# Optimization experiments

Measured on AMD Instinct MI355X. Metric: run time of the kernel, lower is better.

Reference implementation:

```python
import jax, jax.numpy as jnp
import numpy as np

N = 100000   # nodes
E = 1600000  # edges (before self-loops)
G = 64       # graphs in batch
IN = 8
H = 4        # heads
EPS_BN = 1e-5

def setup_inputs() -> dict:
    key = jax.random.key(0)
    ks = jax.random.split(key, 30)
    def nrm(k, shape, s=0.1):
        return jax.random.normal(k, shape, dtype=jnp.float32) * s
    inp = {}
    inp['x'] = nrm(ks[0], (N, IN), 1.0)
    inp['edge_index'] = jax.random.randint(ks[1], (2, E), 0, N)
    inp['batch'] = jnp.sort(jax.random.randint(ks[2], (N,), 0, G))
    # GATConv 1: 8 -> 64, 4 heads (concat=False)
    inp['W1'] = nrm(ks[3], (IN, H * 64)); inp['aS1'] = nrm(ks[4], (H, 64)); inp['aD1'] = nrm(ks[5], (H, 64)); inp['b1'] = jnp.zeros((64,), jnp.float32)
    inp['g1'] = jnp.ones((64,), jnp.float32); inp['be1'] = jnp.zeros((64,), jnp.float32)
    # GATConv 2: 64 -> 64
    inp['W2'] = nrm(ks[6], (64, H * 64)); inp['aS2'] = nrm(ks[7], (H, 64)); inp['aD2'] = nrm(ks[8], (H, 64)); inp['b2'] = jnp.zeros((64,), jnp.float32)
    inp['g2'] = jnp.ones((64,), jnp.float32); inp['be2'] = jnp.zeros((64,), jnp.float32)
    # GATConv 3: 64 -> 32
    inp['W3'] = nrm(ks[9], (64, H * 32)); inp['aS3'] = nrm(ks[10], (H, 32)); inp['aD3'] = nrm(ks[11], (H, 32)); inp['b3'] = jnp.zeros((32,), jnp.float32)
    inp['g3'] = jnp.ones((32,), jnp.float32); inp['be3'] = jnp.zeros((32,), jnp.float32)
    # predictor MLP 32 -> 16 -> 1
    inp['Wp1'] = nrm(ks[12], (32, 16)); inp['bp1'] = jnp.zeros((16,), jnp.float32)
    inp['Wp2'] = nrm(ks[13], (16, 1)); inp['bp2'] = jnp.zeros((1,), jnp.float32)
    return inp

def gat_layer(x, src, dst, W, a_src, a_dst, bias, D):
    # x: [N, Fin]; src/dst: [E'] (self-loops included). PyG GATConv semantics.
    h = (x @ W).reshape(N, H, D)                       # [N,H,D]
    alpha_s = jnp.einsum('nhd,hd->nh', h, a_src)       # [N,H]
    alpha_d = jnp.einsum('nhd,hd->nh', h, a_dst)
    e = jax.nn.leaky_relu(alpha_s[src] + alpha_d[dst], 0.2)  # [E',H]
    # segment softmax over incoming edges of each target node
    m = jax.ops.segment_max(e, dst, num_segments=N)
    e = jnp.exp(e - m[dst])
    s = jax.ops.segment_sum(e, dst, num_segments=N)
    alpha = e / (s[dst] + 1e-16)                       # [E',H]
    out = jax.ops.segment_sum(h[src] * alpha[:, :, None], dst, num_segments=N)  # [N,H,D]
    return out.mean(axis=1) + bias                     # concat=False -> head mean

def batch_norm(x, gamma, beta):
    m = x.mean(0)
    v = x.var(0)
    return (x - m) * jax.lax.rsqrt(v + EPS_BN) * gamma + beta

def reference(x, edge_index, batch,
              W1, aS1, aD1, b1, g1, be1,
              W2, aS2, aD2, b2, g2, be2,
              W3, aS3, aD3, b3, g3, be3,
              Wp1, bp1, Wp2, bp2):
    loop = jnp.arange(N)
    src = jnp.concatenate([edge_index[0], loop])  # add self loops (PyG default)
    dst = jnp.concatenate([edge_index[1], loop])
    h = jax.nn.relu(gat_layer(x, src, dst, W1, aS1, aD1, b1, 64))
    h = batch_norm(h, g1, be1)
    h = jax.nn.relu(gat_layer(h, src, dst, W2, aS2, aD2, b2, 64))
    h = batch_norm(h, g2, be2)
    h = jax.nn.relu(gat_layer(h, src, dst, W3, aS3, aD3, b3, 32))
    h = batch_norm(h, g3, be3)
    # global mean pool over graphs
    cnt = jax.ops.segment_sum(jnp.ones((N,), h.dtype), batch, num_segments=G)
    pooled = jax.ops.segment_sum(h, batch, num_segments=G) / jnp.maximum(cnt, 1.0)[:, None]
    hid = jax.nn.relu(pooled @ Wp1 + bp1)
    return hid @ Wp2 + bp2  # [G,1]
```

## Files before the change

### kernel.cpp

```cpp
#include <hip/hip_runtime.h>
#include <hip/hip_fp16.h>

#define N_NODES 100000
#define N_EDGES 1600000
#define EP (N_EDGES + N_NODES)
#define NG 64
#define NH 4
#define POOL_NPB 256
#define BSHIFT 7
#define BNODES 128
#define NBUCK 782
#define BCAP 3072
#define BCHUNK 4096
#define NBLK2 (N_NODES / 16)
#define NBLK1 (N_NODES / 32)
#define NBINS 64

static inline int cdiv(int a, int b) { return (a + b - 1) / b; }

typedef _Float16 half8 __attribute__((ext_vector_type(8)));
typedef float f32x4 __attribute__((ext_vector_type(4)));

__device__ __forceinline__ float lrelu(float x) { return x >= 0.f ? x : 0.2f * x; }

__global__ __launch_bounds__(256) void k_bucket(const int* __restrict__ ei,
                                                int* __restrict__ gCursor,
                                                unsigned int* __restrict__ pairs) {
  __shared__ int cnt[NBUCK];
  __shared__ int base[NBUCK];
  int tid = threadIdx.x;
  for (int b = tid; b < NBUCK; b += 256) cnt[b] = 0;
  __syncthreads();
  int e0 = blockIdx.x * BCHUNK;
  unsigned int stV[16];
  int stB[16];
#pragma unroll
  for (int i = 0; i < 16; i++) {
    int e = e0 + i * 256 + tid;
    stB[i] = -1;
    if (e < EP) {
      int d, s;
      if (e < N_EDGES) {
        d = __builtin_nontemporal_load(&ei[N_EDGES + e]);
        s = __builtin_nontemporal_load(&ei[e]);
      } else {
        d = s = e - N_EDGES;
      }
      int b = d >> BSHIFT;
      stV[i] = ((unsigned int)s << BSHIFT) | (unsigned int)(d & (BNODES - 1));
      stB[i] = b;
      atomicAdd(&cnt[b], 1);
    }
  }
  __syncthreads();
  for (int b = tid; b < NBUCK; b += 256) {
    base[b] = atomicAdd(&gCursor[b], cnt[b]);
    cnt[b] = 0;
  }
  __syncthreads();
#pragma unroll
  for (int i = 0; i < 16; i++) {
    if (stB[i] >= 0) {
      int r = atomicAdd(&cnt[stB[i]], 1);
      pairs[base[stB[i]] + r] = stV[i];
    }
  }
}

__global__ __launch_bounds__(1024) void k_bscan(const int* __restrict__ gCursor,
                                                int* __restrict__ bstart) {
  __shared__ int sh[1024];
  int t = threadIdx.x;
  int v = (t < NBUCK) ? (gCursor[t] - t * BCAP) : 0;
  sh[t] = v;
  __syncthreads();
  for (int off = 1; off < 1024; off <<= 1) {
    int add = (t >= off) ? sh[t - off] : 0;
    __syncthreads();
    sh[t] += add;
    __syncthreads();
  }
  if (t < NBUCK) {
    bstart[t] = sh[t] - v;
    if (t == NBUCK - 1) bstart[NBUCK] = sh[t];
  }
}

__global__ __launch_bounds__(256) void k_build(const unsigned int* __restrict__ pairs,
                                               const int* __restrict__ bstart,
                                               int* __restrict__ indptr, int* __restrict__ esrc,
                                               int* __restrict__ ghist) {
  __shared__ int cnt[BNODES];
  __shared__ int exc[BNODES];
  __shared__ int ptr[BNODES];
  __shared__ int dh[NBINS];
  __shared__ int eLds[BCAP];
  int b = blockIdx.x;
  int tid = threadIdx.x;
  int obase = bstart[b];
  int nE = bstart[b + 1] - obase;
  int pbase = b * BCAP;
  if (tid < BNODES) cnt[tid] = 0;
  if (tid >= BNODES && tid < BNODES + NBINS) dh[tid - BNODES] = 0;
  __syncthreads();
  unsigned int stV[12];
#pragma unroll
  for (int i = 0; i < 12; i++) {
    int idx = i * 256 + tid;
    stV[i] = 0xFFFFFFFFu;
    if (idx < nE) {
      unsigned int v = pairs[pbase + idx];
      stV[i] = v;
      atomicAdd(&cnt[v & (BNODES - 1)], 1);
    }
  }
  __syncthreads();
  if (tid < BNODES) ptr[tid] = cnt[tid];
  __syncthreads();
  for (int off = 1; off < BNODES; off <<= 1) {
    int add = (tid < BNODES && tid >= off) ? ptr[tid - off] : 0;
    __syncthreads();
    if (tid < BNODES) ptr[tid] += add;
    __syncthreads();
  }
  if (tid < BNODES) {
    exc[tid] = ptr[tid] - cnt[tid];
    int n = (b << BSHIFT) + tid;
    if (n < N_NODES) {
      indptr[n] = obase + exc[tid];
      atomicAdd(&dh[min(cnt[tid], NBINS - 1)], 1);
    }
    cnt[tid] = 0;
  }
  if (b == NBUCK - 1 && tid == 0) indptr[N_NODES] = bstart[NBUCK];
  __syncthreads();
  if (tid < NBINS && dh[tid]) atomicAdd(&ghist[tid], dh[tid]);
#pragma unroll
  for (int i = 0; i < 12; i++) {
    if (stV[i] != 0xFFFFFFFFu) {
      int ln = stV[i] & (BNODES - 1);
      int r = atomicAdd(&cnt[ln], 1);
      eLds[exc[ln] + r] = (int)(stV[i] >> BSHIFT);
    }
  }
  __syncthreads();
  for (int idx = tid; idx < nE; idx += 256) esrc[obase + idx] = eLds[idx];
}

__global__ void k_dscan(const int* __restrict__ ghist, int* __restrict__ binCur) {
  if (threadIdx.x == 0) {
    int acc = 0;
    for (int b = 0; b < NBINS; b++) {
      binCur[b] = acc;
      acc += ghist[b];
    }
  }
}

__global__ __launch_bounds__(256) void k_dscat(const int* __restrict__ indptr,
                                               int* __restrict__ binCur,
                                               int* __restrict__ perm) {
  __shared__ int cnt[NBINS];
  __shared__ int base[NBINS];
  int t = threadIdx.x;
  if (t < NBINS) cnt[t] = 0;
  __syncthreads();
  int binr[2], nr[2];
#pragma unroll
  for (int i = 0; i < 2; i++) {
    int n = blockIdx.x * 512 + i * 256 + t;
    binr[i] = -1;
    if (n < N_NODES) {
      int deg = indptr[n + 1] - indptr[n];
      binr[i] = min(deg, NBINS - 1);
      nr[i] = n;
      atomicAdd(&cnt[binr[i]], 1);
    }
  }
  __syncthreads();
  if (t < NBINS) {
    base[t] = cnt[t] ? atomicAdd(&binCur[t], cnt[t]) : 0;
    cnt[t] = 0;
  }
  __syncthreads();
#pragma unroll
  for (int i = 0; i < 2; i++) {
    if (binr[i] >= 0) {
      int r = atomicAdd(&cnt[binr[i]], 1);
      perm[base[binr[i]] + r] = nr[i];
    }
  }
}

template <int FIN, int D>
__device__ void wvec_impl(const float* __restrict__ W, const float* __restrict__ aS,
                          const float* __restrict__ aD, float* __restrict__ wS,
                          float* __restrict__ wD, int t) {
  if (t >= 4 * FIN) return;
  int h = t / FIN, k = t % FIN;
  float ss = 0.f, dd = 0.f;
  for (int d = 0; d < D; d++) {
    float w = W[k * (4 * D) + h * D + d];
    ss = fmaf(w, aS[h * D + d], ss);
    dd = fmaf(w, aD[h * D + d], dd);
  }
  wS[h * FIN + k] = ss;
  wD[h * FIN + k] = dd;
}

template <int D>
__device__ void wcvt_frag(const float* __restrict__ W, __half* __restrict__ wf, int frag, int l) {
  constexpr int NCT = D / 16;
  int kt = frag / NCT, ct = frag % NCT;
  half8 v;
#pragma unroll
  for (int j = 0; j < 8; j++) {
    int kk = kt * 32 + (l >> 4) * 8 + j;
    int k = kk >> 2, h = kk & 3;
    v[j] = (_Float16)W[k * (4 * D) + h * D + ct * 16 + (l & 15)];
  }
  *(half8*)(wf + (size_t)frag * 512 + l * 8) = v;
}

__global__ __launch_bounds__(256) void k_prep(const float* W1, const float* aS1, const float* aD1,
                                              const float* W2, const float* aS2, const float* aD2,
                                              const float* W3, const float* aS3, const float* aD3,
                                              float* wS1, float* wD1, float* wS2, float* wD2,
                                              float* wS3, float* wD3,
                                              __half* wf1, __half* wf2, __half* wf3,
                                              int* gCursor) {
  int b = blockIdx.x, t = threadIdx.x;
  int f = t >> 6, l = t & 63;
  if (b == 0) wvec_impl<8, 64>(W1, aS1, aD1, wS1, wD1, t);
  else if (b == 1) wvec_impl<64, 64>(W2, aS2, aD2, wS2, wD2, t);
  else if (b == 2) wvec_impl<64, 32>(W3, aS3, aD3, wS3, wD3, t);
  else if (b == 3) wcvt_frag<64>(W1, wf1, f, l);
  else if (b < 12) wcvt_frag<64>(W2, wf2, (b - 4) * 4 + f, l);
  else if (b < 16) wcvt_frag<32>(W3, wf3, (b - 12) * 4 + f, l);
  else {
    int idx = (b - 16) * 256 + t;
    if (idx < NBUCK) gCursor[idx] = idx * BCAP;
  }
}

__global__ void k_attdots1(const float* __restrict__ x, const float* __restrict__ wS,
                           const float* __restrict__ wD, float4* __restrict__ as4,
                           float4* __restrict__ ad4) {
  int n = blockIdx.x * blockDim.x + threadIdx.x;
  if (n >= N_NODES) return;
  float4 s = {0, 0, 0, 0}, d = {0, 0, 0, 0};
#pragma unroll
  for (int k = 0; k < 8; k++) {
    float xv = x[(size_t)n * 8 + k];
    s.x = fmaf(xv, wS[k], s.x);
    s.y = fmaf(xv, wS[8 + k], s.y);
    s.z = fmaf(xv, wS[16 + k], s.z);
    s.w = fmaf(xv, wS[24 + k], s.w);
    d.x = fmaf(xv, wD[k], d.x);
    d.y = fmaf(xv, wD[8 + k], d.y);
    d.z = fmaf(xv, wD[16 + k], d.z);
    d.w = fmaf(xv, wD[24 + k], d.w);
  }
  as4[n] = s;
  ad4[n] = d;
}

__global__ __launch_bounds__(256) void k_dots(const __half* __restrict__ t16,
                                              const float* __restrict__ scale,
                                              const float* __restrict__ shift,
                                              const float* __restrict__ wS,
                                              const float* __restrict__ wD,
                                              float4* __restrict__ as4, float4* __restrict__ ad4) {
  int lane = threadIdx.x & 63;
  int n = blockIdx.x * 4 + (threadIdx.x >> 6);
  if (n >= N_NODES) return;
  float v = fmaf(__half2float(t16[(size_t)n * 64 + lane]), scale[lane], shift[lane]);
  float p0 = v * wS[lane], p1 = v * wS[64 + lane], p2 = v * wS[128 + lane], p3 = v * wS[192 + lane];
  float q0 = v * wD[lane], q1 = v * wD[64 + lane], q2 = v * wD[128 + lane], q3 = v * wD[192 + lane];
#pragma unroll
  for (int off = 32; off; off >>= 1) {
    p0 += __shfl_xor(p0, off); p1 += __shfl_xor(p1, off);
    p2 += __shfl_xor(p2, off); p3 += __shfl_xor(p3, off);
    q0 += __shfl_xor(q0, off); q1 += __shfl_xor(q1, off);
    q2 += __shfl_xor(q2, off); q3 += __shfl_xor(q3, off);
  }
  if (lane == 0) {
    as4[n] = make_float4(p0, p1, p2, p3);
    ad4[n] = make_float4(q0, q1, q2, q3);
  }
}

__global__ __launch_bounds__(256) void k_aggp1(const int* __restrict__ indptr,
                                               const int* __restrict__ perm,
                                               const int* __restrict__ esrc,
                                               const float* __restrict__ xg,
                                               const float4* __restrict__ as4,
                                               const float4* __restrict__ ad4,
                                               const __half* __restrict__ wfrag,
                                               const float* __restrict__ bias,
                                               __half* __restrict__ out16,
                                               float* __restrict__ part) {
  constexpr int GL = 8, NPW = 8, WB = NPW * (GL + 1);
  __shared__ int sOff[4 * WB];
  __shared__ float4 sW[4 * WB];
  __shared__ __align__(16) __half aT[32 * 40];
  int tid = threadIdx.x;
  int lane = tid & 63;
  int wv = tid >> 6;
  int q = lane & 7;
  int g = lane >> 3;
  int row = wv * 8 + g;
  int n = perm[blockIdx.x * 32 + row];
  int e0 = indptr[n], e1 = indptr[n + 1];
  float4 ad = ad4[n];
  int lbase = wv * WB + g * (GL + 1);
  const char* xb = (const char*)xg + q * 4;
  float s0 = 0.f, s1 = 0.f, s2 = 0.f, s3 = 0.f;
  float a0 = 0.f, a1 = 0.f, a2 = 0.f, a3 = 0.f;
  for (int c = e0; c < e1; c += GL) {
    int nc = min(GL, e1 - c);
    float w0 = 0.f, w1 = 0.f, w2 = 0.f, w3 = 0.f;
    int sB = 0;
    if (q < nc) {
      int sidx = esrc[c + q];
      float4 av = as4[sidx];
      w0 = __expf(lrelu(av.x + ad.x));
      w1 = __expf(lrelu(av.y + ad.y));
      w2 = __expf(lrelu(av.z + ad.z));
      w3 = __expf(lrelu(av.w + ad.w));
      sB = sidx << 5;
    }
    s0 += w0; s1 += w1; s2 += w2; s3 += w3;
    sOff[lbase + q] = sB;
    sW[lbase + q] = make_float4(w0, w1, w2, w3);
    __builtin_amdgcn_wave_barrier();
    for (int i = 0; i < nc; ++i) {
      float4 w = sW[lbase + i];
      float xv = *(const float*)(xb + sOff[lbase + i]);
      a0 = fmaf(w.x, xv, a0);
      a1 = fmaf(w.y, xv, a1);
      a2 = fmaf(w.z, xv, a2);
      a3 = fmaf(w.w, xv, a3);
    }
    __builtin_amdgcn_wave_barrier();
  }
#pragma unroll
  for (int off = 1; off < GL; off <<= 1) {
    s0 += __shfl_xor(s0, off);
    s1 += __shfl_xor(s1, off);
    s2 += __shfl_xor(s2, off);
    s3 += __shfl_xor(s3, off);
  }
  float r0 = 1.f / (s0 + 1e-16f), r1 = 1.f / (s1 + 1e-16f);
  float r2 = 1.f / (s2 + 1e-16f), r3 = 1.f / (s3 + 1e-16f);
  __half2 p01 = __floats2half2_rn(a0 * r0, a1 * r1);
  __half2 p23 = __floats2half2_rn(a2 * r2, a3 * r3);
  uint2 pk = make_uint2(*(unsigned*)&p01, *(unsigned*)&p23);
  *(uint2*)&aT[row * 40 + q * 4] = pk;
  __syncthreads();
  int ct = wv;
  int m = lane & 15, kg = lane >> 4;
  half8 bv = *(const half8*)(wfrag + ((size_t)ct * 64 + lane) * 8);
  float bvs = bias[ct * 16 + m];
  float psum = 0.f, psq = 0.f;
#pragma unroll
  for (int tt = 0; tt < 2; tt++) {
    half8 avf = *(const half8*)&aT[(tt * 16 + m) * 40 + kg * 8];
    f32x4 cacc = (f32x4){0.f, 0.f, 0.f, 0.f};
    cacc = __builtin_amdgcn_mfma_f32_16x16x32_f16(avf, bv, cacc, 0, 0, 0);
#pragma unroll
    for (int j = 0; j < 4; j++) {
      int nr = perm[blockIdx.x * 32 + tt * 16 + kg * 4 + j];
      float ov = fmaxf(fmaf(cacc[j], 0.25f, bvs), 0.f);
      out16[(size_t)nr * 64 + ct * 16 + m] = __float2half(ov);
      psum += ov;
      psq = fmaf(ov, ov, psq);
    }
  }
  psum += __shfl_xor(psum, 16); psum += __shfl_xor(psum, 32);
  psq += __shfl_xor(psq, 16); psq += __shfl_xor(psq, 32);
  if (kg == 0) {
    part[(size_t)blockIdx.x * 128 + ct * 16 + m] = psum;
    part[(size_t)blockIdx.x * 128 + 64 + ct * 16 + m] = psq;
  }
}

template <int DOUT, bool OUTH>
__global__ __launch_bounds__(256) void k_aggp(const int* __restrict__ indptr,
                                              const int* __restrict__ perm,
                                              const int* __restrict__ esrc,
                                              const __half* __restrict__ xg,
                                              const float4* __restrict__ as4,
                                              const float4* __restrict__ ad4,
                                              const __half* __restrict__ wfrag,
                                              const float* __restrict__ bias,
                                              const float* __restrict__ scale,
                                              const float* __restrict__ shift,
                                              __half* __restrict__ out16,
                                              float* __restrict__ out32,
                                              float* __restrict__ part) {
  constexpr int NCT = DOUT / 16;
  constexpr int GL = 16, NPW = 4, WB = NPW * (GL + 1);
  __shared__ int sOff[4 * WB];
  __shared__ float4 sW[4 * WB];
  __shared__ __align__(16) __half aT[16 * 264];
  int tid = threadIdx.x;
  int lane = tid & 63;
  int wv = tid >> 6;
  int q = lane & 15;
  int g = lane >> 4;
  int row = wv * 4 + g;
  int n = perm[blockIdx.x * 16 + row];
  int e0 = indptr[n], e1 = indptr[n + 1];
  float4 ad = ad4[n];
  int lbase = wv * WB + g * (GL + 1);
  const char* xb = (const char*)xg + q * 8;
  float s0 = 0.f, s1 = 0.f, s2 = 0.f, s3 = 0.f;
  float a[4][4];
#pragma unroll
  for (int d = 0; d < 4; d++)
#pragma unroll
    for (int h = 0; h < 4; h++) a[d][h] = 0.f;

  for (int c = e0; c < e1; c += GL) {
    int nc = min(GL, e1 - c);
    float w0 = 0.f, w1 = 0.f, w2 = 0.f, w3 = 0.f;
    int sB = 0;
    if (q < nc) {
      int sidx = esrc[c + q];
      float4 av = as4[sidx];
      w0 = __expf(lrelu(av.x + ad.x));
      w1 = __expf(lrelu(av.y + ad.y));
      w2 = __expf(lrelu(av.z + ad.z));
      w3 = __expf(lrelu(av.w + ad.w));
      sB = sidx << 7;
    }
    s0 += w0; s1 += w1; s2 += w2; s3 += w3;
    sOff[lbase + q] = sB;
    sW[lbase + q] = make_float4(w0, w1, w2, w3);
    __builtin_amdgcn_wave_barrier();
    for (int i = 0; i < nc; ++i) {
      float4 w = sW[lbase + i];
      uint2 px = *(const uint2*)(xb + sOff[lbase + i]);
      float2 f01 = __half22float2(*(const __half2*)&px.x);
      float2 f23 = __half22float2(*(const __half2*)&px.y);
      a[0][0] = fmaf(w.x, f01.x, a[0][0]); a[0][1] = fmaf(w.y, f01.x, a[0][1]);
      a[0][2] = fmaf(w.z, f01.x, a[0][2]); a[0][3] = fmaf(w.w, f01.x, a[0][3]);
      a[1][0] = fmaf(w.x, f01.y, a[1][0]); a[1][1] = fmaf(w.y, f01.y, a[1][1]);
      a[1][2] = fmaf(w.z, f01.y, a[1][2]); a[1][3] = fmaf(w.w, f01.y, a[1][3]);
      a[2][0] = fmaf(w.x, f23.x, a[2][0]); a[2][1] = fmaf(w.y, f23.x, a[2][1]);
      a[2][2] = fmaf(w.z, f23.x, a[2][2]); a[2][3] = fmaf(w.w, f23.x, a[2][3]);
      a[3][0] = fmaf(w.x, f23.y, a[3][0]); a[3][1] = fmaf(w.y, f23.y, a[3][1]);
      a[3][2] = fmaf(w.z, f23.y, a[3][2]); a[3][3] = fmaf(w.w, f23.y, a[3][3]);
    }
    __builtin_amdgcn_wave_barrier();
  }
#pragma unroll
  for (int off = 1; off < GL; off <<= 1) {
    s0 += __shfl_xor(s0, off);
    s1 += __shfl_xor(s1, off);
    s2 += __shfl_xor(s2, off);
    s3 += __shfl_xor(s3, off);
  }
  float r0 = 1.f / (s0 + 1e-16f), r1 = 1.f / (s1 + 1e-16f);
  float r2 = 1.f / (s2 + 1e-16f), r3 = 1.f / (s3 + 1e-16f);
  __half2 p[8];
#pragma unroll
  for (int d = 0; d < 4; d++) {
    float sc = scale[q * 4 + d], sh = shift[q * 4 + d];
    p[2 * d] = __floats2half2_rn(fmaf(a[d][0] * r0, sc, sh), fmaf(a[d][1] * r1, sc, sh));
    p[2 * d + 1] = __floats2half2_rn(fmaf(a[d][2] * r2, sc, sh), fmaf(a[d][3] * r3, sc, sh));
  }
  uint4 lo = make_uint4(*(unsigned*)&p[0], *(unsigned*)&p[1], *(unsigned*)&p[2], *(unsigned*)&p[3]);
  uint4 hi = make_uint4(*(unsigned*)&p[4], *(unsigned*)&p[5], *(unsigned*)&p[6], *(unsigned*)&p[7]);
  *(uint4*)&aT[row * 264 + q * 16] = lo;
  *(uint4*)&aT[row * 264 + q * 16 + 8] = hi;
  __syncthreads();
  if (wv < NCT) {
    int ct = wv;
    int m = lane & 15, kg = lane >> 4;
    f32x4 cacc = (f32x4){0.f, 0.f, 0.f, 0.f};
#pragma unroll
    for (int kt = 0; kt < 8; kt++) {
      half8 avf = *(const half8*)&aT[m * 264 + kt * 32 + kg * 8];
      half8 bvf = *(const half8*)(wfrag + ((kt * NCT + ct) * 64 + lane) * 8);
      cacc = __builtin_amdgcn_mfma_f32_16x16x32_f16(avf, bvf, cacc, 0, 0, 0);
    }
    float bv = bias[ct * 16 + m];
    float psum = 0.f, psq = 0.f;
#pragma unroll
    for (int j = 0; j < 4; j++) {
      int nr = perm[blockIdx.x * 16 + kg * 4 + j];
      float ov = fmaxf(fmaf(cacc[j], 0.25f, bv), 0.f);
      if constexpr (OUTH) out16[(size_t)nr * DOUT + ct * 16 + m] = __float2half(ov);
      else out32[(size_t)nr * DOUT + ct * 16 + m] = ov;
      psum += ov;
      psq = fmaf(ov, ov, psq);
    }
    psum += __shfl_xor(psum, 16); psum += __shfl_xor(psum, 32);
    psq += __shfl_xor(psq, 16); psq += __shfl_xor(psq, 32);
    if (kg == 0) {
      part[(size_t)blockIdx.x * (2 * DOUT) + ct * 16 + m] = psum;
      part[(size_t)blockIdx.x * (2 * DOUT) + DOUT + ct * 16 + m] = psq;
    }
  }
}

template <int C>
__global__ __launch_bounds__(256) void k_bnfin2(const float* __restrict__ part, int nb,
                                                const float* __restrict__ g,
                                                const float* __restrict__ be,
                                                float* __restrict__ scale,
                                                float* __restrict__ shift) {
  int c = blockIdx.x;
  int t = threadIdx.x;
  float s = 0.f, q = 0.f;
  for (int b = t; b < nb; b += 256) {
    s += part[(size_t)b * (2 * C) + c];
    q += part[(size_t)b * (2 * C) + C + c];
  }
  __shared__ float sh[512];
  sh[t] = s;
  sh[256 + t] = q;
  __syncthreads();
  for (int step = 128; step; step >>= 1) {
    if (t < step) {
      sh[t] += sh[t + step];
      sh[256 + t] += sh[256 + t + step];
    }
    __syncthreads();
  }
  if (t == 0) {
    float mean = sh[0] / (float)N_NODES;
    float var = sh[256] / (float)N_NODES - mean * mean;
    float sc = g[c] * rsqrtf(var + 1e-5f);
    scale[c] = sc;
    shift[c] = be[c] - mean * sc;
  }
}

__global__ __launch_bounds__(256) void k_pool(const float* __restrict__ f3,
                                              const int* __restrict__ batch,
                                              const float* __restrict__ scale,
                                              const float* __restrict__ shift,
                                              float* __restrict__ pool,
                                              float* __restrict__ cntg) {
  __shared__ float acc[NG][33];
  int t = threadIdx.x;
  for (int i = t; i < NG * 33; i += 256) ((float*)acc)[i] = 0.f;
  __syncthreads();
  int c = t & 31, rg = t >> 5;
  float sc = scale[c], sh = shift[c];
  int n0 = blockIdx.x * POOL_NPB;
  int n1 = min(N_NODES, n0 + POOL_NPB);
  float r = 0.f, rc = 0.f;
  int gcur = -1;
  for (int n = n0 + rg; n < n1; n += 8) {
    int g = batch[n];
    if (g != gcur) {
      if (gcur >= 0) {
        atomicAdd(&acc[gcur][c], r);
        if (c == 0) atomicAdd(&acc[gcur][32], rc);
      }
      gcur = g;
      r = 0.f;
      rc = 0.f;
    }
    r += fmaf(f3[(size_t)n * 32 + c], sc, sh);
    rc += 1.f;
  }
  if (gcur >= 0) {
    atomicAdd(&acc[gcur][c], r);
    if (c == 0) atomicAdd(&acc[gcur][32], rc);
  }
  __syncthreads();
  for (int i = t; i < NG * 32; i += 256) {
    int g = i >> 5, cc = i & 31;
    float v = acc[g][cc];
    if (v != 0.f) atomicAdd(&pool[i], v);
  }
  for (int g = t; g < NG; g += 256) {
    float v = acc[g][32];
    if (v != 0.f) atomicAdd(&cntg[g], v);
  }
}

__global__ void k_mlp(const float* __restrict__ pool, const float* __restrict__ cntg,
                      const float* __restrict__ Wp1, const float* __restrict__ bp1,
                      const float* __restrict__ Wp2, const float* __restrict__ bp2,
                      float* __restrict__ out) {
  int g = threadIdx.x;
  if (g >= NG) return;
  float inv = 1.f / fmaxf(cntg[g], 1.f);
  float p[32];
#pragma unroll
  for (int c = 0; c < 32; c++) p[c] = pool[g * 32 + c] * inv;
  float o = bp2[0];
  for (int j = 0; j < 16; j++) {
    float hsum = bp1[j];
#pragma unroll
    for (int c = 0; c < 32; c++) hsum = fmaf(p[c], Wp1[c * 16 + j], hsum);
    o = fmaf(fmaxf(hsum, 0.f), Wp2[j], o);
  }
  out[g] = o;
}

extern "C" void kernel_launch(void* const* d_in, const int* in_sizes, int n_in,
                              void* d_out, int out_size, void* d_ws, size_t ws_size,
                              hipStream_t stream) {
  const float* x = (const float*)d_in[0];
  const int* ei = (const int*)d_in[1];
  const int* batch = (const int*)d_in[2];
  const float* W1 = (const float*)d_in[3];
  const float* aS1 = (const float*)d_in[4];
  const float* aD1 = (const float*)d_in[5];
  const float* b1 = (const float*)d_in[6];
  const float* g1 = (const float*)d_in[7];
  const float* be1 = (const float*)d_in[8];
  const float* W2 = (const float*)d_in[9];
  const float* aS2 = (const float*)d_in[10];
  const float* aD2 = (const float*)d_in[11];
  const float* b2 = (const float*)d_in[12];
  const float* g2 = (const float*)d_in[13];
  const float* be2 = (const float*)d_in[14];
  const float* W3 = (const float*)d_in[15];
  const float* aS3 = (const float*)d_in[16];
  const float* aD3 = (const float*)d_in[17];
  const float* b3 = (const float*)d_in[18];
  const float* g3 = (const float*)d_in[19];
  const float* be3 = (const float*)d_in[20];
  const float* Wp1 = (const float*)d_in[21];
  const float* bp1 = (const float*)d_in[22];
  const float* Wp2 = (const float*)d_in[23];
  const float* bp2 = (const float*)d_in[24];
  float* out = (float*)d_out;

  size_t off = 0;
  auto alloc = [&](size_t bytes) -> void* {
    void* p = (char*)d_ws + off;
    off += (bytes + 255) & ~(size_t)255;
    return p;
  };
  float* pool = (float*)alloc((size_t)NG * 32 * 4);
  float* cntg = (float*)alloc((size_t)NG * 4);
  int* ghist = (int*)alloc((size_t)NBINS * 4);
  size_t zbytes = off;
  int* gCursor = (int*)alloc((size_t)NBUCK * 4);
  int* bstart = (int*)alloc((size_t)(NBUCK + 1) * 4);
  unsigned int* pairs = (unsigned int*)alloc((size_t)NBUCK * BCAP * 4);
  int* indptr = (int*)alloc((size_t)(N_NODES + 1) * 4);
  int* esrc = (int*)alloc((size_t)EP * 4);
  int* perm = (int*)alloc((size_t)N_NODES * 4);
  int* binCur = (int*)alloc((size_t)NBINS * 4);
  __half* t16a = (__half*)alloc((size_t)N_NODES * 64 * 2);
  __half* t16b = (__half*)alloc((size_t)N_NODES * 64 * 2);
  float* as_ = (float*)alloc((size_t)N_NODES * 16);
  float* ad_ = (float*)alloc((size_t)N_NODES * 16);
  float* tbuf = (float*)alloc((size_t)N_NODES * 32 * 4);
  float* part = (float*)alloc((size_t)NBLK2 * 128 * 4);
  float* scale = (float*)alloc(64 * 4);
  float* shift = (float*)alloc(64 * 4);
  float* wS1 = (float*)alloc(32 * 4);
  float* wD1 = (float*)alloc(32 * 4);
  float* wS2 = (float*)alloc(256 * 4);
  float* wD2 = (float*)alloc(256 * 4);
  float* wS3 = (float*)alloc(256 * 4);
  float* wD3 = (float*)alloc(256 * 4);
  __half* wf1 = (__half*)alloc((size_t)4 * 512 * 2);
  __half* wf2 = (__half*)alloc((size_t)32 * 512 * 2);
  __half* wf3 = (__half*)alloc((size_t)16 * 512 * 2);
  if (off > ws_size) return;

  hipMemsetAsync(pool, 0, zbytes, stream);

  k_prep<<<16 + cdiv(NBUCK, 256), 256, 0, stream>>>(W1, aS1, aD1, W2, aS2, aD2, W3, aS3, aD3,
                                                    wS1, wD1, wS2, wD2, wS3, wD3, wf1, wf2, wf3,
                                                    gCursor);
  k_bucket<<<cdiv(EP, BCHUNK), 256, 0, stream>>>(ei, gCursor, pairs);
  k_bscan<<<1, 1024, 0, stream>>>(gCursor, bstart);
  k_build<<<NBUCK, 256, 0, stream>>>(pairs, bstart, indptr, esrc, ghist);
  k_dscan<<<1, 64, 0, stream>>>(ghist, binCur);
  k_dscat<<<cdiv(N_NODES, 512), 256, 0, stream>>>(indptr, binCur, perm);

  k_attdots1<<<cdiv(N_NODES, 256), 256, 0, stream>>>(x, wS1, wD1, (float4*)as_, (float4*)ad_);
  k_aggp1<<<NBLK1, 256, 0, stream>>>(indptr, perm, esrc, x, (const float4*)as_,
                                     (const float4*)ad_, wf1, b1, t16a, part);
  k_bnfin2<64><<<64, 256, 0, stream>>>(part, NBLK1, g1, be1, scale, shift);

  k_dots<<<cdiv(N_NODES, 4), 256, 0, stream>>>(t16a, scale, shift, wS2, wD2,
                                               (float4*)as_, (float4*)ad_);
  k_aggp<64, true><<<NBLK2, 256, 0, stream>>>(indptr, perm, esrc, t16a, (const float4*)as_,
                                              (const float4*)ad_, wf2, b2, scale, shift,
                                              t16b, nullptr, part);
  k_bnfin2<64><<<64, 256, 0, stream>>>(part, NBLK2, g2, be2, scale, shift);

  k_dots<<<cdiv(N_NODES, 4), 256, 0, stream>>>(t16b, scale, shift, wS3, wD3,
                                               (float4*)as_, (float4*)ad_);
  k_aggp<32, false><<<NBLK2, 256, 0, stream>>>(indptr, perm, esrc, t16b, (const float4*)as_,
                                               (const float4*)ad_, wf3, b3, scale, shift,
                                               nullptr, tbuf, part);
  k_bnfin2<32><<<32, 256, 0, stream>>>(part, NBLK2, g3, be3, scale, shift);

  k_pool<<<cdiv(N_NODES, POOL_NPB), 256, 0, stream>>>(tbuf, batch, scale, shift, pool, cntg);
  k_mlp<<<1, 64, 0, stream>>>(pool, cntg, Wp1, bp1, Wp2, bp2, out);
}
```

Baseline: 377.6 us.

## Renumber nodes into degree-sorted order and rework edge bucketing into larger chunks

Nodes are relabelled into their degree-sorted permuted order. A new k_etrans kernel rewrites edge sources into permuted indices and builds per-position start and end offsets, and x is gathered into permuted order. The aggregation kernels then read and write features, attention dots and edge ranges contiguously by position instead of indirecting through perm, and only the final fp32 output is scattered back to original order. The bucketing kernel now uses four times larger chunks and re-reads the edge indices in a second pass instead of keeping them in registers. This adds an extra pass over all edges and extra buffers in exchange for more regular memory access in the three aggregation layers.

```diff
diff --git a/kernel.cpp b/kernel.cpp
--- a/kernel.cpp
+++ b/kernel.cpp
@@ -11,7 +11,7 @@
 #define BNODES 128
 #define NBUCK 782
 #define BCAP 3072
-#define BCHUNK 4096
+#define BCHUNK 16384
 #define NBLK2 (N_NODES / 16)
 #define NBLK1 (N_NODES / 32)
 #define NBINS 64
@@ -32,38 +32,29 @@
   for (int b = tid; b < NBUCK; b += 256) cnt[b] = 0;
   __syncthreads();
   int e0 = blockIdx.x * BCHUNK;
-  unsigned int stV[16];
-  int stB[16];
-#pragma unroll
-  for (int i = 0; i < 16; i++) {
-    int e = e0 + i * 256 + tid;
-    stB[i] = -1;
-    if (e < EP) {
-      int d, s;
-      if (e < N_EDGES) {
-        d = __builtin_nontemporal_load(&ei[N_EDGES + e]);
-        s = __builtin_nontemporal_load(&ei[e]);
-      } else {
-        d = s = e - N_EDGES;
-      }
-      int b = d >> BSHIFT;
-      stV[i] = ((unsigned int)s << BSHIFT) | (unsigned int)(d & (BNODES - 1));
-      stB[i] = b;
-      atomicAdd(&cnt[b], 1);
-    }
+  int eEnd = min(EP, e0 + BCHUNK);
+  for (int e = e0 + tid; e < eEnd; e += 256) {
+    int d = (e < N_EDGES) ? ei[N_EDGES + e] : (e - N_EDGES);
+    atomicAdd(&cnt[d >> BSHIFT], 1);
   }
   __syncthreads();
   for (int b = tid; b < NBUCK; b += 256) {
-    base[b] = atomicAdd(&gCursor[b], cnt[b]);
+    int c = cnt[b];
+    base[b] = c ? atomicAdd(&gCursor[b], c) : 0;
     cnt[b] = 0;
   }
   __syncthreads();
-#pragma unroll
-  for (int i = 0; i < 16; i++) {
-    if (stB[i] >= 0) {
-      int r = atomicAdd(&cnt[stB[i]], 1);
-      pairs[base[stB[i]] + r] = stV[i];
-    }
+  for (int e = e0 + tid; e < eEnd; e += 256) {
+    int d, s;
+    if (e < N_EDGES) {
+      d = ei[N_EDGES + e];
+      s = ei[e];
+    } else {
+      d = s = e - N_EDGES;
+    }
+    int b = d >> BSHIFT;
+    int r = atomicAdd(&cnt[b], 1);
+    pairs[base[b] + r] = ((unsigned int)s << BSHIFT) | (unsigned int)(d & (BNODES - 1));
   }
 }
 
@@ -159,7 +150,7 @@
 
 __global__ __launch_bounds__(256) void k_dscat(const int* __restrict__ indptr,
                                                int* __restrict__ binCur,
-                                               int* __restrict__ perm) {
+                                               int* __restrict__ perm, int* __restrict__ pinv) {
   __shared__ int cnt[NBINS];
   __shared__ int base[NBINS];
   int t = threadIdx.x;
@@ -187,8 +178,25 @@
   for (int i = 0; i < 2; i++) {
     if (binr[i] >= 0) {
       int r = atomicAdd(&cnt[binr[i]], 1);
-      perm[base[binr[i]] + r] = nr[i];
-    }
+      int pos = base[binr[i]] + r;
+      perm[pos] = nr[i];
+      pinv[nr[i]] = pos;
+    }
+  }
+}
+
+__global__ __launch_bounds__(256) void k_etrans(const int* __restrict__ esrc,
+                                                const int* __restrict__ pinv,
+                                                const int* __restrict__ indptr,
+                                                const int* __restrict__ perm,
+                                                int* __restrict__ esrc2,
+                                                int* __restrict__ stp, int* __restrict__ enp) {
+  int i = blockIdx.x * 256 + threadIdx.x;
+  if (i < EP) esrc2[i] = pinv[esrc[i]];
+  if (i < N_NODES) {
+    int n = perm[i];
+    stp[i] = indptr[n];
+    enp[i] = indptr[n + 1];
   }
 }
 
@@ -243,26 +251,32 @@
   }
 }
 
-__global__ void k_attdots1(const float* __restrict__ x, const float* __restrict__ wS,
-                           const float* __restrict__ wD, float4* __restrict__ as4,
-                           float4* __restrict__ ad4) {
-  int n = blockIdx.x * blockDim.x + threadIdx.x;
-  if (n >= N_NODES) return;
+__global__ void k_prex1(const float* __restrict__ x, const int* __restrict__ perm,
+                        const float* __restrict__ wS, const float* __restrict__ wD,
+                        float* __restrict__ xp, float4* __restrict__ as4,
+                        float4* __restrict__ ad4) {
+  int p = blockIdx.x * blockDim.x + threadIdx.x;
+  if (p >= N_NODES) return;
+  int n = perm[p];
   float4 s = {0, 0, 0, 0}, d = {0, 0, 0, 0};
+  float xv[8];
 #pragma unroll
   for (int k = 0; k < 8; k++) {
-    float xv = x[(size_t)n * 8 + k];
-    s.x = fmaf(xv, wS[k], s.x);
-    s.y = fmaf(xv, wS[8 + k], s.y);
-    s.z = fmaf(xv, wS[16 + k], s.z);
-    s.w = fmaf(xv, wS[24 + k], s.w);
-    d.x = fmaf(xv, wD[k], d.x);
-    d.y = fmaf(xv, wD[8 + k], d.y);
-    d.z = fmaf(xv, wD[16 + k], d.z);
-    d.w = fmaf(xv, wD[24 + k], d.w);
-  }
-  as4[n] = s;
-  ad4[n] = d;
+    xv[k] = x[(size_t)n * 8 + k];
+    s.x = fmaf(xv[k], wS[k], s.x);
+    s.y = fmaf(xv[k], wS[8 + k], s.y);
+    s.z = fmaf(xv[k], wS[16 + k], s.z);
+    s.w = fmaf(xv[k], wS[24 + k], s.w);
+    d.x = fmaf(xv[k], wD[k], d.x);
+    d.y = fmaf(xv[k], wD[8 + k], d.y);
+    d.z = fmaf(xv[k], wD[16 + k], d.z);
+    d.w = fmaf(xv[k], wD[24 + k], d.w);
+  }
+  float4* xpv = (float4*)(xp + (size_t)p * 8);
+  xpv[0] = make_float4(xv[0], xv[1], xv[2], xv[3]);
+  xpv[1] = make_float4(xv[4], xv[5], xv[6], xv[7]);
+  as4[p] = s;
+  ad4[p] = d;
 }
 
 __global__ __launch_bounds__(256) void k_dots(const __half* __restrict__ t16,
@@ -272,9 +286,9 @@
                                               const float* __restrict__ wD,
                                               float4* __restrict__ as4, float4* __restrict__ ad4) {
   int lane = threadIdx.x & 63;
-  int n = blockIdx.x * 4 + (threadIdx.x >> 6);
-  if (n >= N_NODES) return;
-  float v = fmaf(__half2float(t16[(size_t)n * 64 + lane]), scale[lane], shift[lane]);
+  int p = blockIdx.x * 4 + (threadIdx.x >> 6);
+  if (p >= N_NODES) return;
+  float v = fmaf(__half2float(t16[(size_t)p * 64 + lane]), scale[lane], shift[lane]);
   float p0 = v * wS[lane], p1 = v * wS[64 + lane], p2 = v * wS[128 + lane], p3 = v * wS[192 + lane];
   float q0 = v * wD[lane], q1 = v * wD[64 + lane], q2 = v * wD[128 + lane], q3 = v * wD[192 + lane];
 #pragma unroll
@@ -285,15 +299,15 @@
     q2 += __shfl_xor(q2, off); q3 += __shfl_xor(q3, off);
   }
   if (lane == 0) {
-    as4[n] = make_float4(p0, p1, p2, p3);
-    ad4[n] = make_float4(q0, q1, q2, q3);
-  }
-}
-
-__global__ __launch_bounds__(256) void k_aggp1(const int* __restrict__ indptr,
-                                               const int* __restrict__ perm,
-                                               const int* __restrict__ esrc,
-                                               const float* __restrict__ xg,
+    as4[p] = make_float4(p0, p1, p2, p3);
+    ad4[p] = make_float4(q0, q1, q2, q3);
+  }
+}
+
+__global__ __launch_bounds__(256) void k_aggp1(const int* __restrict__ stp,
+                                               const int* __restrict__ enp,
+                                               const int* __restrict__ esrc2,
+                                               const float* __restrict__ xp,
                                                const float4* __restrict__ as4,
                                                const float4* __restrict__ ad4,
                                                const __half* __restrict__ wfrag,
@@ -310,11 +324,11 @@
   int q = lane & 7;
   int g = lane >> 3;
   int row = wv * 8 + g;
-  int n = perm[blockIdx.x * 32 + row];
-  int e0 = indptr[n], e1 = indptr[n + 1];
-  float4 ad = ad4[n];
+  int p = blockIdx.x * 32 + row;
+  int e0 = stp[p], e1 = enp[p];
+  float4 ad = ad4[p];
   int lbase = wv * WB + g * (GL + 1);
-  const char* xb = (const char*)xg + q * 4;
+  const char* xb = (const char*)xp + q * 4;
   float s0 = 0.f, s1 = 0.f, s2 = 0.f, s3 = 0.f;
   float a0 = 0.f, a1 = 0.f, a2 = 0.f, a3 = 0.f;
   for (int c = e0; c < e1; c += GL) {
@@ -322,7 +336,7 @@
     float w0 = 0.f, w1 = 0.f, w2 = 0.f, w3 = 0.f;
     int sB = 0;
     if (q < nc) {
-      int sidx = esrc[c + q];
+      int sidx = esrc2[c + q];
       float4 av = as4[sidx];
       w0 = __expf(lrelu(av.x + ad.x));
       w1 = __expf(lrelu(av.y + ad.y));
@@ -370,9 +384,9 @@
     cacc = __builtin_amdgcn_mfma_f32_16x16x32_f16(avf, bv, cacc, 0, 0, 0);
 #pragma unroll
     for (int j = 0; j < 4; j++) {
-      int nr = perm[blockIdx.x * 32 + tt * 16 + kg * 4 + j];
+      int pr = blockIdx.x * 32 + tt * 16 + kg * 4 + j;
       float ov = fmaxf(fmaf(cacc[j], 0.25f, bvs), 0.f);
-      out16[(size_t)nr * 64 + ct * 16 + m] = __float2half(ov);
+      out16[(size_t)pr * 64 + ct * 16 + m] = __float2half(ov);
       psum += ov;
       psq = fmaf(ov, ov, psq);
     }
@@ -386,9 +400,9 @@
 }
 
 template <int DOUT, bool OUTH>
-__global__ __launch_bounds__(256) void k_aggp(const int* __restrict__ indptr,
-                                              const int* __restrict__ perm,
-                                              const int* __restrict__ esrc,
+__global__ __launch_bounds__(256) void k_aggp(const int* __restrict__ stp,
+                                              const int* __restrict__ enp,
+                                              const int* __restrict__ esrc2,
                                               const __half* __restrict__ xg,
                                               const float4* __restrict__ as4,
                                               const float4* __restrict__ ad4,
@@ -396,6 +410,7 @@
                                               const float* __restrict__ bias,
                                               const float* __restrict__ scale,
                                               const float* __restrict__ shift,
+                                              const int* __restrict__ perm,
                                               __half* __restrict__ out16,
                                               float* __restrict__ out32,
                                               float* __restrict__ part) {
@@ -410,9 +425,9 @@
   int q = lane & 15;
   int g = lane >> 4;
   int row = wv * 4 + g;
-  int n = perm[blockIdx.x * 16 + row];
-  int e0 = indptr[n], e1 = indptr[n + 1];
-  float4 ad = ad4[n];
+  int p = blockIdx.x * 16 + row;
+  int e0 = stp[p], e1 = enp[p];
+  float4 ad = ad4[p];
   int lbase = wv * WB + g * (GL + 1);
   const char* xb = (const char*)xg + q * 8;
   float s0 = 0.f, s1 = 0.f, s2 = 0.f, s3 = 0.f;
@@ -427,7 +442,7 @@
     float w0 = 0.f, w1 = 0.f, w2 = 0.f, w3 = 0.f;
     int sB = 0;
     if (q < nc) {
-      int sidx = esrc[c + q];
+      int sidx = esrc2[c + q];
       float4 av = as4[sidx];
       w0 = __expf(lrelu(av.x + ad.x));
       w1 = __expf(lrelu(av.y + ad.y));
@@ -464,15 +479,15 @@
   }
   float r0 = 1.f / (s0 + 1e-16f), r1 = 1.f / (s1 + 1e-16f);
   float r2 = 1.f / (s2 + 1e-16f), r3 = 1.f / (s3 + 1e-16f);
-  __half2 p[8];
+  __half2 pp[8];
 #pragma unroll
   for (int d = 0; d < 4; d++) {
     float sc = scale[q * 4 + d], sh = shift[q * 4 + d];
-    p[2 * d] = __floats2half2_rn(fmaf(a[d][0] * r0, sc, sh), fmaf(a[d][1] * r1, sc, sh));
-    p[2 * d + 1] = __floats2half2_rn(fmaf(a[d][2] * r2, sc, sh), fmaf(a[d][3] * r3, sc, sh));
-  }
-  uint4 lo = make_uint4(*(unsigned*)&p[0], *(unsigned*)&p[1], *(unsigned*)&p[2], *(unsigned*)&p[3]);
-  uint4 hi = make_uint4(*(unsigned*)&p[4], *(unsigned*)&p[5], *(unsigned*)&p[6], *(unsigned*)&p[7]);
+    pp[2 * d] = __floats2half2_rn(fmaf(a[d][0] * r0, sc, sh), fmaf(a[d][1] * r1, sc, sh));
+    pp[2 * d + 1] = __floats2half2_rn(fmaf(a[d][2] * r2, sc, sh), fmaf(a[d][3] * r3, sc, sh));
+  }
+  uint4 lo = make_uint4(*(unsigned*)&pp[0], *(unsigned*)&pp[1], *(unsigned*)&pp[2], *(unsigned*)&pp[3]);
+  uint4 hi = make_uint4(*(unsigned*)&pp[4], *(unsigned*)&pp[5], *(unsigned*)&pp[6], *(unsigned*)&pp[7]);
   *(uint4*)&aT[row * 264 + q * 16] = lo;
   *(uint4*)&aT[row * 264 + q * 16 + 8] = hi;
   __syncthreads();
@@ -490,10 +505,14 @@
     float psum = 0.f, psq = 0.f;
 #pragma unroll
     for (int j = 0; j < 4; j++) {
-      int nr = perm[blockIdx.x * 16 + kg * 4 + j];
+      int pr = blockIdx.x * 16 + kg * 4 + j;
       float ov = fmaxf(fmaf(cacc[j], 0.25f, bv), 0.f);
-      if constexpr (OUTH) out16[(size_t)nr * DOUT + ct * 16 + m] = __float2half(ov);
-      else out32[(size_t)nr * DOUT + ct * 16 + m] = ov;
+      if constexpr (OUTH) {
+        out16[(size_t)pr * DOUT + ct * 16 + m] = __float2half(ov);
+      } else {
+        int nr = perm[pr];
+        out32[(size_t)nr * DOUT + ct * 16 + m] = ov;
+      }
       psum += ov;
       psq = fmaf(ov, ov, psq);
     }
@@ -650,8 +669,13 @@
   unsigned int* pairs = (unsigned int*)alloc((size_t)NBUCK * BCAP * 4);
   int* indptr = (int*)alloc((size_t)(N_NODES + 1) * 4);
   int* esrc = (int*)alloc((size_t)EP * 4);
+  int* esrc2 = (int*)alloc((size_t)EP * 4);
   int* perm = (int*)alloc((size_t)N_NODES * 4);
+  int* pinv = (int*)alloc((size_t)N_NODES * 4);
+  int* stp = (int*)alloc((size_t)N_NODES * 4);
+  int* enp = (int*)alloc((size_t)N_NODES * 4);
   int* binCur = (int*)alloc((size_t)NBINS * 4);
+  float* xp = (float*)alloc((size_t)N_NODES * 8 * 4);
   __half* t16a = (__half*)alloc((size_t)N_NODES * 64 * 2);
   __half* t16b = (__half*)alloc((size_t)N_NODES * 64 * 2);
   float* as_ = (float*)alloc((size_t)N_NODES * 16);
@@ -680,25 +704,27 @@
   k_bscan<<<1, 1024, 0, stream>>>(gCursor, bstart);
   k_build<<<NBUCK, 256, 0, stream>>>(pairs, bstart, indptr, esrc, ghist);
   k_dscan<<<1, 64, 0, stream>>>(ghist, binCur);
-  k_dscat<<<cdiv(N_NODES, 512), 256, 0, stream>>>(indptr, binCur, perm);
-
-  k_attdots1<<<cdiv(N_NODES, 256), 256, 0, stream>>>(x, wS1, wD1, (float4*)as_, (float4*)ad_);
-  k_aggp1<<<NBLK1, 256, 0, stream>>>(indptr, perm, esrc, x, (const float4*)as_,
+  k_dscat<<<cdiv(N_NODES, 512), 256, 0, stream>>>(indptr, binCur, perm, pinv);
+  k_etrans<<<cdiv(EP, 256), 256, 0, stream>>>(esrc, pinv, indptr, perm, esrc2, stp, enp);
+
+  k_prex1<<<cdiv(N_NODES, 256), 256, 0, stream>>>(x, perm, wS1, wD1, xp,
+                                                  (float4*)as_, (float4*)ad_);
+  k_aggp1<<<NBLK1, 256, 0, stream>>>(stp, enp, esrc2, xp, (const float4*)as_,
                                      (const float4*)ad_, wf1, b1, t16a, part);
   k_bnfin2<64><<<64, 256, 0, stream>>>(part, NBLK1, g1, be1, scale, shift);
 
   k_dots<<<cdiv(N_NODES, 4), 256, 0, stream>>>(t16a, scale, shift, wS2, wD2,
                                                (float4*)as_, (float4*)ad_);
-  k_aggp<64, true><<<NBLK2, 256, 0, stream>>>(indptr, perm, esrc, t16a, (const float4*)as_,
+  k_aggp<64, true><<<NBLK2, 256, 0, stream>>>(stp, enp, esrc2, t16a, (const float4*)as_,
                                               (const float4*)ad_, wf2, b2, scale, shift,
-                                              t16b, nullptr, part);
+                                              perm, t16b, nullptr, part);
   k_bnfin2<64><<<64, 256, 0, stream>>>(part, NBLK2, g2, be2, scale, shift);
 
   k_dots<<<cdiv(N_NODES, 4), 256, 0, stream>>>(t16b, scale, shift, wS3, wD3,
                                                (float4*)as_, (float4*)ad_);
-  k_aggp<32, false><<<NBLK2, 256, 0, stream>>>(indptr, perm, esrc, t16b, (const float4*)as_,
+  k_aggp<32, false><<<NBLK2, 256, 0, stream>>>(stp, enp, esrc2, t16b, (const float4*)as_,
                                                (const float4*)ad_, wf3, b3, scale, shift,
-                                               nullptr, tbuf, part);
+                                               perm, nullptr, tbuf, part);
   k_bnfin2<32><<<32, 256, 0, stream>>>(part, NBLK2, g3, be3, scale, shift);
 
   k_pool<<<cdiv(N_NODES, POOL_NPB), 256, 0, stream>>>(tbuf, batch, scale, shift, pool, cntg);
```

Result: slower. 400.6 us (+6.1%).
